# Optimization experiments

Measured on AMD Instinct MI355X. Metric: run time of the kernel, lower is better.

Reference implementation:

```python
import jax, jax.numpy as jnp
import numpy as np

L = 4          # decomposition_levels
PRUNE_Q = 0.4  # pruning_ratio


def haar_dwt2(img):
    a = img[:, 0::2, 0::2]; b = img[:, 0::2, 1::2]
    c = img[:, 1::2, 0::2]; d = img[:, 1::2, 1::2]
    cA = (a + b + c + d) * 0.5
    cH = (a - b + c - d) * 0.5
    cV = (a + b - c - d) * 0.5
    cD = (a - b - c + d) * 0.5
    return cA, cH, cV, cD


def haar_idwt2(cA, cH, cV, cD):
    # exact inverse of haar_dwt2: [B, h, w] -> [B, 2h, 2w]
    a = (cA + cH + cV + cD) * 0.5
    b = (cA - cH + cV - cD) * 0.5
    c = (cA + cH - cV - cD) * 0.5
    d = (cA - cH - cV + cD) * 0.5
    B, h, w = cA.shape
    top = jnp.stack([a, b], axis=-1).reshape(B, h, 2 * w)  # interleave cols
    bot = jnp.stack([c, d], axis=-1).reshape(B, h, 2 * w)
    return jnp.stack([top, bot], axis=2).reshape(B, 2 * h, 2 * w)  # interleave rows


def setup_inputs() -> dict:
    key = jax.random.key(0)
    k1, k2, k3 = jax.random.split(key, 3)
    B, in_dim, out_dim = 128, 4096, 4096
    x = jax.random.normal(k1, (B, in_dim), jnp.float32)
    base_weight = jax.random.normal(k2, (out_dim, in_dim), jnp.float32) * 0.02
    bias = jax.random.normal(k3, (out_dim,), jnp.float32) * 0.02
    scale_factors = jnp.ones((L, 4), jnp.float32)  # per-level, per-subband
    return {"x": x, "base_weight": base_weight, "bias": bias,
            "scale_factors": scale_factors}


def reference(x, base_weight, bias, scale_factors):
    B, in_dim = x.shape
    S = int(np.sqrt(in_dim))  # 64: each sample viewed as SxS image
    base_out = x @ base_weight.T  # [B, out_dim]

    # multi-level Haar analysis with per-level scaling + quantile pruning
    cA = x.reshape(B, S, S)
    levels = []
    for l in range(L):
        cA, cH, cV, cD = haar_dwt2(cA)
        co = jnp.stack([cA, cH, cV, cD], axis=1)  # [B, 4, h, w]
        co = co * scale_factors[l][None, :, None, None]
        ab = jnp.abs(co)
        thr = jnp.quantile(ab, PRUNE_Q, axis=-1, keepdims=True)
        co = co * (ab > thr).astype(co.dtype)
        levels.append(co)

    # synthesis from pruned coefficients
    rec = levels[-1][:, 0]  # coarsest pruned cA
    for l in range(L - 1, -1, -1):
        rec = haar_idwt2(rec, levels[l][:, 1], levels[l][:, 2], levels[l][:, 3])

    wavelet_out = rec.reshape(B, in_dim)  # out_dim == in_dim
    return base_out + wavelet_out + bias
```

## Files before the change

### kernel.cpp

```cpp
#include <hip/hip_runtime.h>
#include <hip/hip_bf16.h>

typedef __attribute__((ext_vector_type(8))) short bf16x8;
typedef __attribute__((ext_vector_type(4))) float f32x4;

__device__ __forceinline__ unsigned short f2bf(float f) {
  unsigned int u = __float_as_uint(f);
  u += 0x7FFFu + ((u >> 16) & 1u);
  return (unsigned short)(u >> 16);
}

__device__ __forceinline__ bf16x8 pack8(float4 lo, float4 hi) {
  union { unsigned int u[4]; bf16x8 v; } r;
  asm("v_cvt_pk_bf16_f32 %0, %1, %2" : "=v"(r.u[0]) : "v"(lo.x), "v"(lo.y));
  asm("v_cvt_pk_bf16_f32 %0, %1, %2" : "=v"(r.u[1]) : "v"(lo.z), "v"(lo.w));
  asm("v_cvt_pk_bf16_f32 %0, %1, %2" : "=v"(r.u[2]) : "v"(hi.x), "v"(hi.y));
  asm("v_cvt_pk_bf16_f32 %0, %1, %2" : "=v"(r.u[3]) : "v"(hi.z), "v"(hi.w));
  return r.v;
}

__device__ __forceinline__ void gload16(const void* g, void* l) {
  __builtin_amdgcn_global_load_lds(
      (const __attribute__((address_space(1))) void*)g,
      (__attribute__((address_space(3))) void*)l, 16, 0, 0);
}

__host__ __device__ constexpr int prOffset(int l) {
  return (l == 0) ? 0 : (l == 1) ? 3072 : (l == 2) ? 3840 : 4032;
}

__global__ __launch_bounds__(256) void cvt_x(const float* __restrict__ x,
                                             unsigned short* __restrict__ xb) {
  const int i = blockIdx.x * 256 + threadIdx.x;
  const float4 v = ((const float4*)x)[i];
  ushort4 pk = {f2bf(v.x), f2bf(v.y), f2bf(v.z), f2bf(v.w)};
  ((ushort4*)xb)[i] = pk;
}

template<int L>
__device__ __forceinline__ void level_fwd(float* cur, float* tmp, float* ab,
                                          float* pr, float* thrL, float* thrH,
                                          const float* __restrict__ scl, int tid) {
  constexpr int HALF = 32 >> L, LOG2 = 5 - L, HH = HALF * HALF, TOT = 4 * HH;
  constexpr int H = HALF * 2;
  constexpr int ST = HALF + 4;
  constexpr float P = 0.4f * (float)(HALF - 1);
  constexpr int K = (int)P;
  constexpr float FRAC = P - (float)K;
  const float s0 = scl[4 * L + 0], s1 = scl[4 * L + 1];
  const float s2 = scl[4 * L + 2], s3 = scl[4 * L + 3];
  for (int e = tid; e < HH; e += 1024) {
    const int i = e >> LOG2, j = e & (HALF - 1);
    const float a = cur[(i * 2) * H + j * 2];
    const float b = cur[(i * 2) * H + j * 2 + 1];
    const float c = cur[(i * 2 + 1) * H + j * 2];
    const float d = cur[(i * 2 + 1) * H + j * 2 + 1];
    const float vA = (((a + b) + c) + d) * 0.5f;
    const float vH = (((a - b) + c) - d) * 0.5f;
    const float vV = (((a + b) - c) - d) * 0.5f;
    const float vD = (((a - b) - c) + d) * 0.5f;
    tmp[e]          = vA;  ab[(0 * HALF + i) * ST + j] = fabsf(vA * s0);
    tmp[HH + e]     = vH;  ab[(1 * HALF + i) * ST + j] = fabsf(vH * s1);
    tmp[2 * HH + e] = vV;  ab[(2 * HALF + i) * ST + j] = fabsf(vV * s2);
    tmp[3 * HH + e] = vD;  ab[(3 * HALF + i) * ST + j] = fabsf(vD * s3);
  }
  __syncthreads();
  constexpr int CH = (TOT >= 1024) ? TOT / 1024 : 1;
  {
    const int base = tid * CH;
    if (base < TOT) {
      const int row = base >> LOG2;
      const int c0 = base & (HALF - 1);
      const float* rp = &ab[row * ST];
      float v[CH]; int clt[CH], ceq[CH];
#pragma unroll
      for (int c = 0; c < CH; ++c) { v[c] = rp[c0 + c]; clt[c] = 0; ceq[c] = 0; }
#pragma unroll
      for (int rq = 0; rq < HALF / 4; ++rq) {
        const float4 q = *(const float4*)&rp[rq * 4];
        float qa[4] = {q.x, q.y, q.z, q.w};
#pragma unroll
        for (int z = 0; z < 4; ++z) {
#pragma unroll
          for (int c = 0; c < CH; ++c) {
            clt[c] += (qa[z] < v[c]) ? 1 : 0;
            ceq[c] += (qa[z] == v[c]) ? 1 : 0;
          }
        }
      }
#pragma unroll
      for (int c = 0; c < CH; ++c) {
        if (clt[c] <= K && K < clt[c] + ceq[c]) thrL[row] = v[c];
        if (clt[c] <= K + 1 && K + 1 < clt[c] + ceq[c]) thrH[row] = v[c];
      }
    }
  }
  __syncthreads();
  for (int e = tid; e < TOT; e += 1024) {
    const int s = e >> (2 * LOG2);
    const int row = e >> LOG2;
    const float sc = (s < 2) ? (s == 0 ? s0 : s1) : (s == 2 ? s2 : s3);
    const float thr = thrL[row] * (1.0f - FRAC) + thrH[row] * FRAC;
    const float co = tmp[e] * sc;
    const float val = (fabsf(co) > thr) ? co : 0.0f;
    if (s >= 1) pr[prOffset(L) + e - HH] = val;
    else {
      if (L == 3) pr[4080 + e] = val;
      cur[e] = tmp[e];
    }
  }
  __syncthreads();
}

__global__ __launch_bounds__(1024) void wavelet_kernel(
    const float* __restrict__ x, const float* __restrict__ bias,
    const float* __restrict__ scl, float* __restrict__ out,
    const float* __restrict__ partials, int addPartials) {
  __shared__ __align__(16) float sh[16384];
  float* cur = sh;
  float* tmp = sh + 4096;
  float* ab  = sh + 8192;
  float* pr  = sh + 12288;
  float* thrL = cur + 2048;
  float* thrH = cur + 2176;
  const int b = blockIdx.x, tid = threadIdx.x;
  const float* xi = x + (size_t)b * 4096;

  for (int i = tid; i < 1024; i += 1024)
    *(float4*)&cur[i * 4] = ((const float4*)xi)[i];
  __syncthreads();

  level_fwd<0>(cur, tmp, ab, pr, thrL, thrH, scl, tid);
  level_fwd<1>(cur, tmp, ab, pr, thrL, thrH, scl, tid);
  level_fwd<2>(cur, tmp, ab, pr, thrL, thrH, scl, tid);
  level_fwd<3>(cur, tmp, ab, pr, thrL, thrH, scl, tid);

#pragma unroll
  for (int l = 3; l >= 0; --l) {
    const int half = 64 >> (l + 1);
    const int hh = half * half;
    const int po = prOffset(l);
    const float* src = (l == 3) ? &pr[4080] : ((l & 1) ? tmp : cur);
    float* dst = (l & 1) ? cur : tmp;
    const int W2 = half * 2;
    for (int e = tid; e < hh; e += 1024) {
      const int i = e / half, j = e - i * half;
      const float cA = src[e];
      const float cH = pr[po + 0 * hh + i * half + j];
      const float cV = pr[po + 1 * hh + i * half + j];
      const float cD = pr[po + 2 * hh + i * half + j];
      const float a2 = (((cA + cH) + cV) + cD) * 0.5f;
      const float b2 = (((cA - cH) + cV) - cD) * 0.5f;
      const float c2 = (((cA + cH) - cV) - cD) * 0.5f;
      const float d2 = (((cA - cH) - cV) + cD) * 0.5f;
      dst[(i * 2) * W2 + j * 2]         = a2;
      dst[(i * 2) * W2 + j * 2 + 1]     = b2;
      dst[(i * 2 + 1) * W2 + j * 2]     = c2;
      dst[(i * 2 + 1) * W2 + j * 2 + 1] = d2;
    }
    __syncthreads();
  }
  float* o = out + (size_t)b * 4096;
  const float4* t4 = (const float4*)tmp;
  const float4* b4 = (const float4*)bias;
  for (int i = tid; i < 1024; i += 1024) {
    float4 t = t4[i], bb = b4[i];
    float4 s = {t.x + bb.x, t.y + bb.y, t.z + bb.z, t.w + bb.w};
    if (addPartials) {
#pragma unroll
      for (int ks = 0; ks < 8; ++ks) {
        const float4 p = *(const float4*)&partials[(size_t)ks * 524288 +
                                                   (size_t)b * 4096 + i * 4];
        s.x += p.x; s.y += p.y; s.z += p.z; s.w += p.w;
      }
    }
    ((float4*)o)[i] = s;
  }
}

__global__ __launch_bounds__(256, 4) void gemm_v5(
    const unsigned short* __restrict__ xb, const float* __restrict__ w,
    float* __restrict__ partials) {
  __shared__ __align__(16) unsigned short A_lds[2][128 * 32];
  __shared__ __align__(16) float B_lds[2][64 * 32];
  const int tid = threadIdx.x, lane = tid & 63, wv = tid >> 6;
  const int fr = lane & 15, kq = lane >> 4;
  const int nt = blockIdx.x & 63, ks = blockIdx.x >> 6;
  const int n0 = nt * 64, k0 = ks * 512;

  const int sA0 = tid, sA1 = 256 + tid;
  const int rA0 = sA0 >> 2, cA0 = (sA0 & 3) ^ ((rA0 >> 1) & 3);
  const int rA1 = sA1 >> 2, cA1 = (sA1 & 3) ^ ((rA1 >> 1) & 3);
  const unsigned short* aSrc0 = xb + (size_t)rA0 * 4096 + k0 + cA0 * 8;
  const unsigned short* aSrc1 = xb + (size_t)rA1 * 4096 + k0 + cA1 * 8;
  const int rB0 = sA0 >> 3, cB0 = (sA0 & 7) ^ (rB0 & 7);
  const int rB1 = sA1 >> 3, cB1 = (sA1 & 7) ^ (rB1 & 7);
  const float* bSrc0 = w + (size_t)(n0 + rB0) * 4096 + k0 + cB0 * 4;
  const float* bSrc1 = w + (size_t)(n0 + rB1) * 4096 + k0 + cB1 * 4;

  f32x4 acc[8];
#pragma unroll
  for (int mi = 0; mi < 8; ++mi) acc[mi] = f32x4{0.f, 0.f, 0.f, 0.f};

  const int aslot = kq ^ ((fr >> 1) & 3);
  const int R2 = wv * 16 + fr;
  const int bo0 = R2 * 128 + (((kq * 2 + 0) ^ (R2 & 7)) * 16);
  const int bo1 = R2 * 128 + (((kq * 2 + 1) ^ (R2 & 7)) * 16);

  auto STAGE = [&](int buf, int t) {
    gload16(aSrc0 + t * 32, (char*)&A_lds[buf][0] + tid * 16);
    gload16(aSrc1 + t * 32, (char*)&A_lds[buf][0] + (256 + tid) * 16);
    gload16(bSrc0 + t * 32, (char*)&B_lds[buf][0] + tid * 16);
    gload16(bSrc1 + t * 32, (char*)&B_lds[buf][0] + (256 + tid) * 16);
  };

  STAGE(0, 0);
  __syncthreads();
  int cur = 0;
#pragma unroll
  for (int t = 0; t < 16; ++t) {
    if (t < 15) STAGE(cur ^ 1, t + 1);
    const char* Ab = (const char*)&A_lds[cur][0];
    const char* Bb = (const char*)&B_lds[cur][0];
    const float4 b0 = *(const float4*)(Bb + bo0);
    const float4 b1 = *(const float4*)(Bb + bo1);
    const bf16x8 bb = pack8(b0, b1);
#pragma unroll
    for (int mi = 0; mi < 8; ++mi) {
      const bf16x8 af = *(const bf16x8*)(Ab + (mi * 16 + fr) * 64 + aslot * 16);
      acc[mi] = __builtin_amdgcn_mfma_f32_16x16x32_bf16(af, bb, acc[mi], 0, 0, 0);
    }
    __syncthreads();
    cur ^= 1;
  }

  float* P = partials + (size_t)ks * 524288;
  const int col = n0 + wv * 16 + fr;
  const int rq = kq * 4;
#pragma unroll
  for (int mi = 0; mi < 8; ++mi)
#pragma unroll
    for (int j = 0; j < 4; ++j)
      P[(size_t)(mi * 16 + rq + j) * 4096 + col] = acc[mi][j];
}

__global__ __launch_bounds__(256, 2) void gemm_kernel(
    const float* __restrict__ x, const float* __restrict__ w,
    float* __restrict__ out) {
  __shared__ __align__(16) unsigned short Asm[2][128][40];
  __shared__ __align__(16) unsigned short Bsm[2][64][40];
  const int tid = threadIdx.x;
  const int nt = blockIdx.x & 63, ks = blockIdx.x >> 6;
  const int n0 = nt * 64, k0 = ks * 512;
  const int q = tid & 7, r0 = tid >> 3;
  const int lane = tid & 63, wid = tid >> 6;
  const int wm = wid >> 1, wn = wid & 1;
  const int fr = lane & 15, k8 = (lane >> 4) * 8;

  f32x4 acc[4][2];
#pragma unroll
  for (int mi = 0; mi < 4; ++mi)
#pragma unroll
    for (int ni = 0; ni < 2; ++ni) acc[mi][ni] = f32x4{0.f, 0.f, 0.f, 0.f};

  float4 ra[4]; float4 rb[2];
#pragma unroll
  for (int p = 0; p < 4; ++p)
    ra[p] = *(const float4*)&x[(size_t)(r0 + p * 32) * 4096 + k0 + q * 4];
#pragma unroll
  for (int p = 0; p < 2; ++p)
    rb[p] = *(const float4*)&w[(size_t)(n0 + r0 + p * 32) * 4096 + k0 + q * 4];
#pragma unroll
  for (int p = 0; p < 4; ++p) {
    ushort4 pk = {f2bf(ra[p].x), f2bf(ra[p].y), f2bf(ra[p].z), f2bf(ra[p].w)};
    *(ushort4*)&Asm[0][r0 + p * 32][q * 4] = pk;
  }
#pragma unroll
  for (int p = 0; p < 2; ++p) {
    ushort4 pk = {f2bf(rb[p].x), f2bf(rb[p].y), f2bf(rb[p].z), f2bf(rb[p].w)};
    *(ushort4*)&Bsm[0][r0 + p * 32][q * 4] = pk;
  }
  __syncthreads();

  for (int t = 0; t < 16; ++t) {
    const int cb2 = t & 1;
    if (t < 15) {
      const int kg = k0 + (t + 1) * 32;
#pragma unroll
      for (int p = 0; p < 4; ++p)
        ra[p] = *(const float4*)&x[(size_t)(r0 + p * 32) * 4096 + kg + q * 4];
#pragma unroll
      for (int p = 0; p < 2; ++p)
        rb[p] = *(const float4*)&w[(size_t)(n0 + r0 + p * 32) * 4096 + kg + q * 4];
    }
    bf16x8 af[4], bg[2];
#pragma unroll
    for (int mi = 0; mi < 4; ++mi)
      af[mi] = *(const bf16x8*)&Asm[cb2][wm * 64 + mi * 16 + fr][k8];
#pragma unroll
    for (int ni = 0; ni < 2; ++ni)
      bg[ni] = *(const bf16x8*)&Bsm[cb2][wn * 32 + ni * 16 + fr][k8];
#pragma unroll
    for (int mi = 0; mi < 4; ++mi)
#pragma unroll
      for (int ni = 0; ni < 2; ++ni)
        acc[mi][ni] = __builtin_amdgcn_mfma_f32_16x16x32_bf16(af[mi], bg[ni],
                                                              acc[mi][ni], 0, 0, 0);
    if (t < 15) {
#pragma unroll
      for (int p = 0; p < 4; ++p) {
        ushort4 pk = {f2bf(ra[p].x), f2bf(ra[p].y), f2bf(ra[p].z), f2bf(ra[p].w)};
        *(ushort4*)&Asm[cb2 ^ 1][r0 + p * 32][q * 4] = pk;
      }
#pragma unroll
      for (int p = 0; p < 2; ++p) {
        ushort4 pk = {f2bf(rb[p].x), f2bf(rb[p].y), f2bf(rb[p].z), f2bf(rb[p].w)};
        *(ushort4*)&Bsm[cb2 ^ 1][r0 + p * 32][q * 4] = pk;
      }
    }
    __syncthreads();
  }

  const int rbase = wm * 64 + (lane >> 4) * 4;
  const int cbase = n0 + wn * 32 + fr;
#pragma unroll
  for (int mi = 0; mi < 4; ++mi)
#pragma unroll
    for (int ni = 0; ni < 2; ++ni)
#pragma unroll
      for (int j = 0; j < 4; ++j)
        atomicAdd(&out[(size_t)(rbase + mi * 16 + j) * 4096 + cbase + ni * 16],
                  acc[mi][ni][j]);
}

extern "C" void kernel_launch(void* const* d_in, const int* in_sizes, int n_in,
                              void* d_out, int out_size, void* d_ws, size_t ws_size,
                              hipStream_t stream) {
  const float* x    = (const float*)d_in[0];
  const float* w    = (const float*)d_in[1];
  const float* bias = (const float*)d_in[2];
  const float* scl  = (const float*)d_in[3];
  float* out = (float*)d_out;
  unsigned short* xbp = (unsigned short*)d_ws;
  float* partials = (float*)((char*)d_ws + (1 << 20));
  const size_t need = (1u << 20) + 8u * 524288u * 4u;
  if (ws_size >= need) {
    hipLaunchKernelGGL(cvt_x, dim3(512), dim3(256), 0, stream, x, xbp);
    hipLaunchKernelGGL(gemm_v5, dim3(512), dim3(256), 0, stream, xbp, w, partials);
    hipLaunchKernelGGL(wavelet_kernel, dim3(128), dim3(1024), 0, stream,
                       x, bias, scl, out, partials, 1);
  } else {
    hipLaunchKernelGGL(wavelet_kernel, dim3(128), dim3(1024), 0, stream,
                       x, bias, scl, out, (const float*)nullptr, 0);
    hipLaunchKernelGGL(gemm_kernel, dim3(512), dim3(256), 0, stream, x, w, out);
  }
}
```

Baseline: 126.0 us.

## Compute quantile thresholds with wavefront shuffles instead of LDS rank pass

Replaces the per-row rank counting over a padded LDS array, which wrote thresholds to shared memory and needed an extra barrier, with a wavefront-local approach. Each lane loads its value, counts smaller and equal values in its row via __shfl, and the row's two order statistics are combined with an xor-shuffle max reduction. The pruning and store step is folded into the same loop, removing one __syncthreads per level and the threshold arrays. The cost is more shuffle instructions per element, where the old code reused one rank pass across several elements per thread.

```diff
diff --git a/kernel.cpp b/kernel.cpp
--- a/kernel.cpp
+++ b/kernel.cpp
@@ -39,11 +39,10 @@
 
 template<int L>
 __device__ __forceinline__ void level_fwd(float* cur, float* tmp, float* ab,
-                                          float* pr, float* thrL, float* thrH,
+                                          float* pr,
                                           const float* __restrict__ scl, int tid) {
   constexpr int HALF = 32 >> L, LOG2 = 5 - L, HH = HALF * HALF, TOT = 4 * HH;
   constexpr int H = HALF * 2;
-  constexpr int ST = HALF + 4;
   constexpr float P = 0.4f * (float)(HALF - 1);
   constexpr int K = (int)P;
   constexpr float FRAC = P - (float)K;
@@ -59,54 +58,44 @@
     const float vH = (((a - b) + c) - d) * 0.5f;
     const float vV = (((a + b) - c) - d) * 0.5f;
     const float vD = (((a - b) - c) + d) * 0.5f;
-    tmp[e]          = vA;  ab[(0 * HALF + i) * ST + j] = fabsf(vA * s0);
-    tmp[HH + e]     = vH;  ab[(1 * HALF + i) * ST + j] = fabsf(vH * s1);
-    tmp[2 * HH + e] = vV;  ab[(2 * HALF + i) * ST + j] = fabsf(vV * s2);
-    tmp[3 * HH + e] = vD;  ab[(3 * HALF + i) * ST + j] = fabsf(vD * s3);
-  }
-  __syncthreads();
-  constexpr int CH = (TOT >= 1024) ? TOT / 1024 : 1;
+    tmp[e]          = vA;  ab[e]          = fabsf(vA * s0);
+    tmp[HH + e]     = vH;  ab[HH + e]     = fabsf(vH * s1);
+    tmp[2 * HH + e] = vV;  ab[2 * HH + e] = fabsf(vV * s2);
+    tmp[3 * HH + e] = vD;  ab[3 * HH + e] = fabsf(vD * s3);
+  }
+  __syncthreads();
   {
-    const int base = tid * CH;
-    if (base < TOT) {
-      const int row = base >> LOG2;
-      const int c0 = base & (HALF - 1);
-      const float* rp = &ab[row * ST];
-      float v[CH]; int clt[CH], ceq[CH];
-#pragma unroll
-      for (int c = 0; c < CH; ++c) { v[c] = rp[c0 + c]; clt[c] = 0; ceq[c] = 0; }
-#pragma unroll
-      for (int rq = 0; rq < HALF / 4; ++rq) {
-        const float4 q = *(const float4*)&rp[rq * 4];
-        float qa[4] = {q.x, q.y, q.z, q.w};
-#pragma unroll
-        for (int z = 0; z < 4; ++z) {
-#pragma unroll
-          for (int c = 0; c < CH; ++c) {
-            clt[c] += (qa[z] < v[c]) ? 1 : 0;
-            ceq[c] += (qa[z] == v[c]) ? 1 : 0;
-          }
-        }
-      }
-#pragma unroll
-      for (int c = 0; c < CH; ++c) {
-        if (clt[c] <= K && K < clt[c] + ceq[c]) thrL[row] = v[c];
-        if (clt[c] <= K + 1 && K + 1 < clt[c] + ceq[c]) thrH[row] = v[c];
-      }
-    }
-  }
-  __syncthreads();
-  for (int e = tid; e < TOT; e += 1024) {
-    const int s = e >> (2 * LOG2);
-    const int row = e >> LOG2;
-    const float sc = (s < 2) ? (s == 0 ? s0 : s1) : (s == 2 ? s2 : s3);
-    const float thr = thrL[row] * (1.0f - FRAC) + thrH[row] * FRAC;
-    const float co = tmp[e] * sc;
-    const float val = (fabsf(co) > thr) ? co : 0.0f;
-    if (s >= 1) pr[prOffset(L) + e - HH] = val;
-    else {
-      if (L == 3) pr[4080 + e] = val;
-      cur[e] = tmp[e];
+    const int lane = tid & 63, wvi = tid >> 6;
+    constexpr int NTASK = TOT / 64;
+    const int idx = lane & (HALF - 1);
+    const int laneBase = lane & ~(HALF - 1);
+    for (int task = wvi; task < NTASK; task += 16) {
+      const int e = task * 64 + lane;
+      const float v = ab[e];
+      int clt = 0, ceq = 1;
+#pragma unroll
+      for (int s = 1; s < HALF; ++s) {
+        const float u = __shfl(v, laneBase + ((idx + s) & (HALF - 1)), 64);
+        clt += (u < v) ? 1 : 0;
+        ceq += (u == v) ? 1 : 0;
+      }
+      float vlo = (clt <= K && K < clt + ceq) ? v : 0.0f;
+      float vhi = (clt <= K + 1 && K + 1 < clt + ceq) ? v : 0.0f;
+#pragma unroll
+      for (int m = HALF / 2; m >= 1; m >>= 1) {
+        vlo = fmaxf(vlo, __shfl_xor(vlo, m, 64));
+        vhi = fmaxf(vhi, __shfl_xor(vhi, m, 64));
+      }
+      const float thr = vlo * (1.0f - FRAC) + vhi * FRAC;
+      const int sb = e >> (2 * LOG2);
+      const float sc = (sb < 2) ? (sb == 0 ? s0 : s1) : (sb == 2 ? s2 : s3);
+      const float co = tmp[e] * sc;
+      const float val = (v > thr) ? co : 0.0f;
+      if (sb >= 1) pr[prOffset(L) + e - HH] = val;
+      else {
+        if (L == 3) pr[4080 + e] = val;
+        cur[e] = tmp[e];
+      }
     }
   }
   __syncthreads();
@@ -121,8 +110,6 @@
   float* tmp = sh + 4096;
   float* ab  = sh + 8192;
   float* pr  = sh + 12288;
-  float* thrL = cur + 2048;
-  float* thrH = cur + 2176;
   const int b = blockIdx.x, tid = threadIdx.x;
   const float* xi = x + (size_t)b * 4096;
 
@@ -130,10 +117,10 @@
     *(float4*)&cur[i * 4] = ((const float4*)xi)[i];
   __syncthreads();
 
-  level_fwd<0>(cur, tmp, ab, pr, thrL, thrH, scl, tid);
-  level_fwd<1>(cur, tmp, ab, pr, thrL, thrH, scl, tid);
-  level_fwd<2>(cur, tmp, ab, pr, thrL, thrH, scl, tid);
-  level_fwd<3>(cur, tmp, ab, pr, thrL, thrH, scl, tid);
+  level_fwd<0>(cur, tmp, ab, pr, scl, tid);
+  level_fwd<1>(cur, tmp, ab, pr, scl, tid);
+  level_fwd<2>(cur, tmp, ab, pr, scl, tid);
+  level_fwd<3>(cur, tmp, ab, pr, scl, tid);
 
 #pragma unroll
   for (int l = 3; l >= 0; --l) {
```

Measured after the change: 127.7 us. About the same (+1.3%).
